# Kernel optimization log

Measured on AMD Instinct MI355X. Metric: run time of the kernel, lower is better.

The kernel has to match this reference:

```python
import jax, jax.numpy as jnp
import numpy as np

EPS = 1e-8  # torch F.cosine_similarity default eps


def setup_inputs() -> dict:
    key = jax.random.key(0)
    k1, k2 = jax.random.split(key)
    x = jax.random.normal(k1, (16384, 1024), dtype=jnp.float32)
    label = jax.random.randint(k2, (16384, 64), 0, 2).astype(jnp.int64)
    w = jnp.asarray(10.0, dtype=jnp.float32)  # nn.Parameter init_w
    b = jnp.asarray(-5.0, dtype=jnp.float32)  # nn.Parameter init_b
    return {"x": x, "label": label, "w": w, "b": b}


def reference(x, label, w, b):
    # Append the 'no-label' column for rows whose label vector is all zero.
    extra = (label.sum(axis=1) == 0).astype(label.dtype)[:, None]
    lab = jnp.concatenate([label, extra], axis=1).astype(x.dtype)  # [B, C]

    counts = lab.sum(axis=0)                  # [C] positives per centroid
    active = counts > 0                       # torch drops empty columns; we mask them

    # Centroids: mean of x over rows carrying each label (scatter-mean as GEMM).
    anchor = (lab.T @ x) / jnp.maximum(counts, 1.0)[:, None]   # [C, D]

    # Cosine similarity between every sample and every centroid.
    xn = jnp.maximum(jnp.linalg.norm(x, axis=1), EPS)          # [B]
    an = jnp.maximum(jnp.linalg.norm(anchor, axis=1), EPS)     # [C]
    cos = (x @ anchor.T) / (xn[:, None] * an[None, :])          # [B, C]

    logits = cos * w + b
    # Removing empty columns from softmax == setting their logits to -inf.
    logits = jnp.where(active[None, :], logits, -jnp.inf)
    logp = jax.nn.log_softmax(logits, axis=1)                   # [B, C]

    # Row expansion in torch duplicates sample i once per positive label j;
    # the logits row only depends on i, so CE over expanded rows is a
    # pair-weighted mean of -logp[i, j] over positive (i, j) pairs.
    n_pairs = lab.sum()
    nloss = -jnp.sum(jnp.where(lab > 0, logp, 0.0)) / n_pairs
    return nloss
```

## Files before the change

kernel.cpp:

```cpp
#include <hip/hip_runtime.h>
#include <hip/hip_bf16.h>
#include <stdint.h>

#define NROWS 16384
#define NDIM  1024
#define NLAB  64
#define NC    65
#define CPAD  80

typedef float float4v __attribute__((ext_vector_type(4)));
typedef short short8  __attribute__((ext_vector_type(8)));

static constexpr size_t SCALE_B = 0;
static constexpr size_t ACTB_B  = 320;
static constexpr size_t WSUM_B  = 400;
static constexpr size_t CNTF_B  = 448;
static constexpr size_t CNTP_B  = 1024;
static constexpr size_t MASK_B  = 83968;
static constexpr size_t XN2_B   = 215040;
static constexpr size_t LFRAG_B = 280576;
static constexpr size_t BFRAG_B = 2902016;
static constexpr size_t XAF_B   = 3065856;
static constexpr size_t PART_B  = 70174720;
static constexpr size_t SLAB    = (size_t)CPAD * NDIM * 4;
static constexpr size_t ANCH_SZ = (size_t)CPAD * NDIM * 4;
static constexpr size_t NRM_SZ  = (size_t)CPAD * 4 * 4;

__device__ __forceinline__ unsigned short bf16u(float f) {
    __hip_bfloat16 h = __float2bfloat16(f);
    return __builtin_bit_cast(unsigned short, h);
}
__device__ __forceinline__ unsigned pk2(float a, float b) {
    return (unsigned)bf16u(a) | ((unsigned)bf16u(b) << 16);
}

__global__ __launch_bounds__(256, 4) void k01_prep(const float* __restrict__ x,
                                                   const int* __restrict__ label,
                                                   unsigned short* __restrict__ xAfrag,
                                                   float* __restrict__ xn2g,
                                                   unsigned long long* __restrict__ masks,
                                                   unsigned* __restrict__ cntpart,
                                                   unsigned short* __restrict__ lfrag) {
    __shared__ unsigned cnt[NC];
    __shared__ unsigned long long smask[64];
    __shared__ float red[4][16];
    int t = threadIdx.x;
    if (blockIdx.x < 1024) {
        int rt = blockIdx.x;
        int w = t >> 6, lane = t & 63, q = lane >> 4, col = lane & 15;
        const float* rowp = x + ((size_t)rt * 16 + col) * NDIM;
        uint4* dst = (uint4*)xAfrag + ((size_t)rt * 32 + w * 8) * 64 + lane;
        float sq = 0.f;
#pragma unroll
        for (int kb = 0; kb < 8; ++kb) {
            int d0 = w * 256 + kb * 32 + q * 8;
            float4 fa = *(const float4*)(rowp + d0);
            float4 fb = *(const float4*)(rowp + d0 + 4);
            sq += fa.x * fa.x + fa.y * fa.y + fa.z * fa.z + fa.w * fa.w
                + fb.x * fb.x + fb.y * fb.y + fb.z * fb.z + fb.w * fb.w;
            uint4 v;
            v.x = pk2(fa.x, fa.y); v.y = pk2(fa.z, fa.w);
            v.z = pk2(fb.x, fb.y); v.w = pk2(fb.z, fb.w);
            dst[kb * 64] = v;
        }
        sq += __shfl_xor(sq, 16, 64);
        sq += __shfl_xor(sq, 32, 64);
        if (q == 0) red[w][col] = sq;
        __syncthreads();
        if (t < 16) xn2g[rt * 16 + t] = red[0][t] + red[1][t] + red[2][t] + red[3][t];
        return;
    }
    int bid = blockIdx.x - 1024;
    if (t < NC) cnt[t] = 0;
    __syncthreads();
    int wave = t >> 6, lane = t & 63;
    int rowblock = bid * 64;
    unsigned creg = 0, zreg = 0;
#pragma unroll 4
    for (int p = 0; p < 16; ++p) {
        int row = rowblock + p * 4 + wave;
        int v = label[row * NLAB + lane];
        unsigned long long m = __ballot(v != 0);
        creg += (unsigned)((m >> lane) & 1ull);
        if (lane == 0) {
            masks[row] = m;
            smask[p * 4 + wave] = m;
            zreg += (m == 0ull) ? 1u : 0u;
        }
    }
    atomicAdd(&cnt[lane], creg);
    if (lane == 0 && zreg) atomicAdd(&cnt[64], zreg);
    __syncthreads();
    if (t < 80) cntpart[bid * 80 + t] = (t < NC) ? cnt[t] : 0u;
    for (int pid = t; pid < 640; pid += 256) {
        int rt2l = pid / 320, rem = pid % 320;
        int ct = rem >> 6, ln = rem & 63;
        int q = ln >> 4, col = ln & 15;
        int c = ct * 16 + col;
        int rbase = rt2l * 32 + q * 8;
        unsigned pk[4];
#pragma unroll
        for (int jp = 0; jp < 4; ++jp) {
            unsigned long long m0 = smask[rbase + jp * 2], m1 = smask[rbase + jp * 2 + 1];
            unsigned b0, b1;
            if (c < 64)       { b0 = (unsigned)((m0 >> c) & 1ull); b1 = (unsigned)((m1 >> c) & 1ull); }
            else if (c == 64) { b0 = (m0 == 0ull); b1 = (m1 == 0ull); }
            else              { b0 = 0u; b1 = 0u; }
            pk[jp] = (b0 ? 0x3F80u : 0u) | (b1 ? 0x3F800000u : 0u);
        }
        uint4 w = make_uint4(pk[0], pk[1], pk[2], pk[3]);
        ((uint4*)lfrag)[((size_t)(bid * 2 + rt2l) * 5 + ct) * 64 + ln] = w;
    }
}

__global__ __launch_bounds__(256) void k2_sums(const float* __restrict__ x,
                                               const unsigned short* __restrict__ lfrag,
                                               float* __restrict__ partial,
                                               int kslices) {
    int t = threadIdx.x, wave = t >> 6, lane = t & 63;
    int q = lane >> 4, col = lane & 15;
    int dgroup = blockIdx.x & 15, ks = blockIdx.x >> 4;
    int nkb = (NROWS / kslices) >> 5;
    int kb0 = ks * nkb;
    int d = dgroup * 64 + wave * 16 + col;
    const uint4* A = (const uint4*)lfrag;
    const float* xb = x + d;

    float4v acc[5];
#pragma unroll
    for (int ct = 0; ct < 5; ++ct) acc[ct] = (float4v){0.f, 0.f, 0.f, 0.f};

    float f0[8], f1[8];
    uint4 a0[5], a1[5];
    {
        const float* p = xb + (size_t)(kb0 * 32 + q * 8) * NDIM;
#pragma unroll
        for (int j = 0; j < 8; ++j) f0[j] = p[(size_t)j * NDIM];
#pragma unroll
        for (int ct = 0; ct < 5; ++ct) a0[ct] = A[((size_t)kb0 * 5 + ct) * 64 + lane];
        const float* p1 = xb + (size_t)((kb0 + 1) * 32 + q * 8) * NDIM;
#pragma unroll
        for (int j = 0; j < 8; ++j) f1[j] = p1[(size_t)j * NDIM];
#pragma unroll
        for (int ct = 0; ct < 5; ++ct) a1[ct] = A[((size_t)(kb0 + 1) * 5 + ct) * 64 + lane];
    }

    for (int i = 0; i < nkb; i += 2) {
        int p2 = i + 2 < nkb ? kb0 + i + 2 : kb0 + i;
        int p3 = i + 3 < nkb ? kb0 + i + 3 : kb0 + i + 1;
        {
            uint4 bq;
            bq.x = pk2(f0[0], f0[1]); bq.y = pk2(f0[2], f0[3]);
            bq.z = pk2(f0[4], f0[5]); bq.w = pk2(f0[6], f0[7]);
            short8 bf = __builtin_bit_cast(short8, bq);
#pragma unroll
            for (int ct = 0; ct < 5; ++ct) {
                short8 af = __builtin_bit_cast(short8, a0[ct]);
                acc[ct] = __builtin_amdgcn_mfma_f32_16x16x32_bf16(af, bf, acc[ct], 0, 0, 0);
            }
            const float* p = xb + (size_t)(p2 * 32 + q * 8) * NDIM;
#pragma unroll
            for (int j = 0; j < 8; ++j) f0[j] = p[(size_t)j * NDIM];
#pragma unroll
            for (int ct = 0; ct < 5; ++ct) a0[ct] = A[((size_t)p2 * 5 + ct) * 64 + lane];
        }
        {
            uint4 bq;
            bq.x = pk2(f1[0], f1[1]); bq.y = pk2(f1[2], f1[3]);
            bq.z = pk2(f1[4], f1[5]); bq.w = pk2(f1[6], f1[7]);
            short8 bf = __builtin_bit_cast(short8, bq);
#pragma unroll
            for (int ct = 0; ct < 5; ++ct) {
                short8 af = __builtin_bit_cast(short8, a1[ct]);
                acc[ct] = __builtin_amdgcn_mfma_f32_16x16x32_bf16(af, bf, acc[ct], 0, 0, 0);
            }
            const float* p = xb + (size_t)(p3 * 32 + q * 8) * NDIM;
#pragma unroll
            for (int j = 0; j < 8; ++j) f1[j] = p[(size_t)j * NDIM];
#pragma unroll
            for (int ct = 0; ct < 5; ++ct) a1[ct] = A[((size_t)p3 * 5 + ct) * 64 + lane];
        }
    }
    float* pb = partial + (size_t)ks * CPAD * NDIM;
#pragma unroll
    for (int ct = 0; ct < 5; ++ct)
#pragma unroll
        for (int reg = 0; reg < 4; ++reg)
            pb[(size_t)(ct * 16 + q * 4 + reg) * NDIM + d] = acc[ct][reg];
}

__global__ __launch_bounds__(256) void k2bA(const float* __restrict__ partial,
                                            int kslices,
                                            float* __restrict__ anchor_raw,
                                            float* __restrict__ norm2part) {
    __shared__ float red[4];
    int c = blockIdx.x >> 2, dq = blockIdx.x & 3, t = threadIdx.x;
    int d = dq * 256 + t;
    const float* p = partial + (size_t)c * NDIM + d;
    float s = 0.f;
#pragma unroll 8
    for (int sl = 0; sl < kslices; ++sl) s += p[(size_t)sl * CPAD * NDIM];
    anchor_raw[(size_t)c * NDIM + d] = s;
    float ss = s * s;
#pragma unroll
    for (int m = 32; m >= 1; m >>= 1) ss += __shfl_xor(ss, m, 64);
    if ((t & 63) == 0) red[t >> 6] = ss;
    __syncthreads();
    if (t == 0) norm2part[blockIdx.x] = red[0] + red[1] + red[2] + red[3];
}

__global__ __launch_bounds__(1024) void k2bB(const float* __restrict__ wptr,
                                             const unsigned* __restrict__ cntpart,
                                             const float* __restrict__ anchor_raw,
                                             const float* __restrict__ norm2part,
                                             unsigned short* __restrict__ bfrag,
                                             float* __restrict__ scale,
                                             unsigned char* __restrict__ actB,
                                             unsigned* __restrict__ countsF,
                                             float* __restrict__ wsum) {
    int c = blockIdx.x, t = threadIdx.x;
    __shared__ float red[16];
    __shared__ unsigned credu[4];
    __shared__ float bcast[1];
    if (c == 0 && t == 512) *wsum = 0.f;
    if (t < 256) {
        unsigned cv = cntpart[t * 80 + c];
#pragma unroll
        for (int m = 32; m >= 1; m >>= 1) cv += __shfl_xor(cv, m, 64);
        if ((t & 63) == 0) credu[t >> 6] = cv;
    }
    if (t == 0)
        bcast[0] = sqrtf(norm2part[c * 4] + norm2part[c * 4 + 1] +
                         norm2part[c * 4 + 2] + norm2part[c * 4 + 3]);
    __syncthreads();
    unsigned cnt = credu[0] + credu[1] + credu[2] + credu[3];
    float invc = 1.0f / (float)(cnt > 0u ? cnt : 1u);
    float a = anchor_raw[(size_t)c * NDIM + t] * invc;
    float an = fmaxf(bcast[0] * invc, 1e-8f);
    unsigned short h = bf16u(a / an);
    int ct = c >> 4, colc = c & 15;
    int kb = t >> 5, q = (t >> 3) & 3, j0 = t & 7;
    bfrag[((((size_t)ct * 32 + kb) * 64) + q * 16 + colc) * 8 + j0] = h;
    float hv = __bfloat162float(__builtin_bit_cast(__hip_bfloat16, h));
    float nb2 = hv * hv;
#pragma unroll
    for (int m = 32; m >= 1; m >>= 1) nb2 += __shfl_xor(nb2, m, 64);
    if ((t & 63) == 0) red[t >> 6] = nb2;
    __syncthreads();
    if (t == 0) {
        float n2 = 0.f;
#pragma unroll
        for (int j = 0; j < 16; ++j) n2 += red[j];
        scale[c] = (n2 > 0.f) ? (wptr[0] / sqrtf(n2)) : 0.f;
        actB[c] = (cnt > 0u) ? 1 : 0;
        countsF[c] = cnt;
    }
}

__global__ __launch_bounds__(256) void k3_loss(const unsigned short* __restrict__ xAfrag,
                                               const unsigned short* __restrict__ bfrag,
                                               const float* __restrict__ xn2g,
                                               const unsigned long long* __restrict__ masks,
                                               const unsigned char* __restrict__ actB,
                                               const float* __restrict__ scale,
                                               const float* __restrict__ bptr,
                                               float* __restrict__ wsum) {
    __shared__ float redsm[3][64][21];
    int t = threadIdx.x, wave = t >> 6, lane = t & 63;
    int q = lane >> 4, col = lane & 15;
    int rt = blockIdx.x;
    int rowbase = rt * 16;
    const uint4* A = (const uint4*)xAfrag + (size_t)rt * 32 * 64 + lane;
    const uint4* Bp = (const uint4*)bfrag + lane;
    int kb0 = wave * 8;

    float4v acc[5];
#pragma unroll
    for (int ct = 0; ct < 5; ++ct) acc[ct] = (float4v){0.f, 0.f, 0.f, 0.f};

    uint4 a0 = A[(size_t)(kb0 + 0) * 64], a1 = A[(size_t)(kb0 + 1) * 64];
    uint4 b0[5], b1[5];
#pragma unroll
    for (int ct = 0; ct < 5; ++ct) b0[ct] = Bp[(size_t)(ct * 32 + kb0 + 0) * 64];
#pragma unroll
    for (int ct = 0; ct < 5; ++ct) b1[ct] = Bp[(size_t)(ct * 32 + kb0 + 1) * 64];

    for (int s = 0; s < 8; s += 2) {
        int p2 = s + 2 < 8 ? kb0 + s + 2 : kb0 + s;
        int p3 = s + 3 < 8 ? kb0 + s + 3 : kb0 + s + 1;
        {
            short8 af = __builtin_bit_cast(short8, a0);
#pragma unroll
            for (int ct = 0; ct < 5; ++ct) {
                short8 bf = __builtin_bit_cast(short8, b0[ct]);
                acc[ct] = __builtin_amdgcn_mfma_f32_16x16x32_bf16(af, bf, acc[ct], 0, 0, 0);
            }
            a0 = A[(size_t)p2 * 64];
#pragma unroll
            for (int ct = 0; ct < 5; ++ct) b0[ct] = Bp[(size_t)(ct * 32 + p2) * 64];
        }
        {
            short8 af = __builtin_bit_cast(short8, a1);
#pragma unroll
            for (int ct = 0; ct < 5; ++ct) {
                short8 bf = __builtin_bit_cast(short8, b1[ct]);
                acc[ct] = __builtin_amdgcn_mfma_f32_16x16x32_bf16(af, bf, acc[ct], 0, 0, 0);
            }
            a1 = A[(size_t)p3 * 64];
#pragma unroll
            for (int ct = 0; ct < 5; ++ct) b1[ct] = Bp[(size_t)(ct * 32 + p3) * 64];
        }
    }

    if (wave) {
#pragma unroll
        for (int ct = 0; ct < 5; ++ct)
#pragma unroll
            for (int reg = 0; reg < 4; ++reg)
                redsm[wave - 1][lane][ct * 4 + reg] = acc[ct][reg];
    }
    __syncthreads();
    if (wave != 0) return;
#pragma unroll
    for (int w = 0; w < 3; ++w)
#pragma unroll
        for (int ct = 0; ct < 5; ++ct)
#pragma unroll
            for (int reg = 0; reg < 4; ++reg)
                acc[ct][reg] += redsm[w][lane][ct * 4 + reg];

    float bv = bptr[0];
    float sc[5]; unsigned char ab[5];
#pragma unroll
    for (int ct = 0; ct < 5; ++ct) { sc[ct] = scale[ct * 16 + col]; ab[ct] = actB[ct * 16 + col]; }

    float contrib = 0.f;
#pragma unroll
    for (int reg = 0; reg < 4; ++reg) {
        int rl = q * 4 + reg;
        int row = rowbase + rl;
        float inv = 1.0f / fmaxf(sqrtf(xn2g[row]), 1e-8f);
        unsigned long long mask = masks[row];
        float v[5]; float lmax = -1e30f;
#pragma unroll
        for (int ct = 0; ct < 5; ++ct) {
            float lg = acc[ct][reg] * sc[ct] * inv + bv;
            v[ct] = ab[ct] ? lg : -1e30f;
            lmax = fmaxf(lmax, v[ct]);
        }
#pragma unroll
        for (int m = 1; m < 16; m <<= 1) lmax = fmaxf(lmax, __shfl_xor(lmax, m, 16));
        float es = 0.f;
#pragma unroll
        for (int ct = 0; ct < 5; ++ct) es += expf(v[ct] - lmax);
#pragma unroll
        for (int m = 1; m < 16; m <<= 1) es += __shfl_xor(es, m, 16);
        float lse = lmax + logf(es);
        float ps = 0.f;
#pragma unroll
        for (int ct = 0; ct < 5; ++ct) {
            int c = ct * 16 + col;
            bool pos = (c < 64) ? (((mask >> c) & 1ull) != 0ull)
                                : ((c == 64) ? (mask == 0ull) : false);
            ps += pos ? v[ct] : 0.f;
        }
#pragma unroll
        for (int m = 1; m < 16; m <<= 1) ps += __shfl_xor(ps, m, 16);
        float npos = mask ? (float)__popcll(mask) : 1.0f;
        float crow = ps - npos * lse;
        if (col == 0) contrib += crow;
    }
#pragma unroll
    for (int m = 1; m < 64; m <<= 1) contrib += __shfl_xor(contrib, m, 64);
    if (lane == 0) atomicAdd(wsum, contrib);
}

__global__ void k4_final(const unsigned* __restrict__ countsF,
                         const float* __restrict__ wsum,
                         float* __restrict__ out) {
    if (threadIdx.x == 0 && blockIdx.x == 0) {
        float np = 0.f;
        for (int c = 0; c < NC; ++c) np += (float)countsF[c];
        out[0] = -wsum[0] / np;
    }
}

extern "C" void kernel_launch(void* const* d_in, const int* in_sizes, int n_in,
                              void* d_out, int out_size, void* d_ws, size_t ws_size,
                              hipStream_t stream) {
    (void)in_sizes; (void)n_in; (void)out_size;
    const float* x = (const float*)d_in[0];
    const int* label = (const int*)d_in[1];
    const float* w = (const float*)d_in[2];
    const float* b = (const float*)d_in[3];

    char* ws = (char*)d_ws;
    float* scale = (float*)(ws + SCALE_B);
    unsigned char* actB = (unsigned char*)(ws + ACTB_B);
    float* wsum = (float*)(ws + WSUM_B);
    unsigned* countsF = (unsigned*)(ws + CNTF_B);
    unsigned* cntpart = (unsigned*)(ws + CNTP_B);
    unsigned long long* masks = (unsigned long long*)(ws + MASK_B);
    float* xn2g = (float*)(ws + XN2_B);
    unsigned short* lfrag = (unsigned short*)(ws + LFRAG_B);
    unsigned short* bfrag = (unsigned short*)(ws + BFRAG_B);
    unsigned short* xAfrag = (unsigned short*)(ws + XAF_B);
    float* partial = (float*)(ws + PART_B);

    int kslices = 64;
    while (kslices > 8 && PART_B + (size_t)kslices * SLAB + ANCH_SZ + NRM_SZ > ws_size)
        kslices >>= 1;
    float* anchor_raw = (float*)(ws + PART_B + (size_t)kslices * SLAB);
    float* norm2part = anchor_raw + CPAD * NDIM;

    hipLaunchKernelGGL(k01_prep, dim3(1024 + 256), dim3(256), 0, stream,
                       x, label, xAfrag, xn2g, masks, cntpart, lfrag);
    hipLaunchKernelGGL(k2_sums, dim3(16 * kslices), dim3(256), 0, stream,
                       x, lfrag, partial, kslices);
    hipLaunchKernelGGL(k2bA, dim3(CPAD * 4), dim3(256), 0, stream,
                       partial, kslices, anchor_raw, norm2part);
    hipLaunchKernelGGL(k2bB, dim3(CPAD), dim3(1024), 0, stream,
                       w, cntpart, anchor_raw, norm2part, bfrag, scale, actB, countsF, wsum);
    hipLaunchKernelGGL(k3_loss, dim3(NROWS / 16), dim3(256), 0, stream,
                       xAfrag, bfrag, xn2g, masks, actB, scale, b, wsum);
    hipLaunchKernelGGL(k4_final, dim3(1), dim3(64), 0, stream, countsF, wsum, (float*)d_out);
}
```

Baseline: 168.5 us.

## Fuse slice-reduction kernels, fold final into loss, stage x tile through LDS

Several independent changes land together. The two-stage partial reduction (k2bA + k2bB) becomes a single kC_fuse kernel. k4_final is folded into k3_loss with a last-block-done counter. kB_sums now loads x rows coalesced into a double-buffered LDS tile instead of issuing strided per-column global loads. The prep kernel batches all x loads before computing and drops its occupancy hint. These aim to cut launch count and uncoalesced traffic, at the cost of a per-iteration barrier in the sums loop and a serialized partial-sum read in the fused kernel (80 blocks each reading kslices slabs).

```diff
diff --git a/kernel.cpp b/kernel.cpp
--- a/kernel.cpp
+++ b/kernel.cpp
@@ -14,6 +14,7 @@
 static constexpr size_t SCALE_B = 0;
 static constexpr size_t ACTB_B  = 320;
 static constexpr size_t WSUM_B  = 400;
+static constexpr size_t DONE_B  = 404;
 static constexpr size_t CNTF_B  = 448;
 static constexpr size_t CNTP_B  = 1024;
 static constexpr size_t MASK_B  = 83968;
@@ -21,10 +22,8 @@
 static constexpr size_t LFRAG_B = 280576;
 static constexpr size_t BFRAG_B = 2902016;
 static constexpr size_t XAF_B   = 3065856;
-static constexpr size_t PART_B  = 70174720;
+static constexpr size_t PART_B  = 36620288;
 static constexpr size_t SLAB    = (size_t)CPAD * NDIM * 4;
-static constexpr size_t ANCH_SZ = (size_t)CPAD * NDIM * 4;
-static constexpr size_t NRM_SZ  = (size_t)CPAD * 4 * 4;
 
 __device__ __forceinline__ unsigned short bf16u(float f) {
     __hip_bfloat16 h = __float2bfloat16(f);
@@ -34,46 +33,50 @@
     return (unsigned)bf16u(a) | ((unsigned)bf16u(b) << 16);
 }
 
-__global__ __launch_bounds__(256, 4) void k01_prep(const float* __restrict__ x,
-                                                   const int* __restrict__ label,
-                                                   unsigned short* __restrict__ xAfrag,
-                                                   float* __restrict__ xn2g,
-                                                   unsigned long long* __restrict__ masks,
-                                                   unsigned* __restrict__ cntpart,
-                                                   unsigned short* __restrict__ lfrag) {
+__global__ __launch_bounds__(256) void kP_prep(const float* __restrict__ x,
+                                               const int* __restrict__ label,
+                                               unsigned short* __restrict__ xAfrag,
+                                               float* __restrict__ xn2g,
+                                               unsigned long long* __restrict__ masks,
+                                               unsigned* __restrict__ cntpart,
+                                               unsigned short* __restrict__ lfrag) {
+    __shared__ float red2[4][16];
     __shared__ unsigned cnt[NC];
     __shared__ unsigned long long smask[64];
-    __shared__ float red[4][16];
     int t = threadIdx.x;
+    int wave = t >> 6, lane = t & 63;
+    int q = lane >> 4, col = lane & 15;
     if (blockIdx.x < 1024) {
         int rt = blockIdx.x;
-        int w = t >> 6, lane = t & 63, q = lane >> 4, col = lane & 15;
         const float* rowp = x + ((size_t)rt * 16 + col) * NDIM;
-        uint4* dst = (uint4*)xAfrag + ((size_t)rt * 32 + w * 8) * 64 + lane;
+        uint4* dst = (uint4*)xAfrag + ((size_t)rt * 32 + wave * 8) * 64 + lane;
+        float4 fa[8], fb[8];
+#pragma unroll
+        for (int kb = 0; kb < 8; ++kb) {
+            int d0 = wave * 256 + kb * 32 + q * 8;
+            fa[kb] = *(const float4*)(rowp + d0);
+            fb[kb] = *(const float4*)(rowp + d0 + 4);
+        }
         float sq = 0.f;
 #pragma unroll
         for (int kb = 0; kb < 8; ++kb) {
-            int d0 = w * 256 + kb * 32 + q * 8;
-            float4 fa = *(const float4*)(rowp + d0);
-            float4 fb = *(const float4*)(rowp + d0 + 4);
-            sq += fa.x * fa.x + fa.y * fa.y + fa.z * fa.z + fa.w * fa.w
-                + fb.x * fb.x + fb.y * fb.y + fb.z * fb.z + fb.w * fb.w;
+            sq += fa[kb].x * fa[kb].x + fa[kb].y * fa[kb].y + fa[kb].z * fa[kb].z + fa[kb].w * fa[kb].w
+                + fb[kb].x * fb[kb].x + fb[kb].y * fb[kb].y + fb[kb].z * fb[kb].z + fb[kb].w * fb[kb].w;
             uint4 v;
-            v.x = pk2(fa.x, fa.y); v.y = pk2(fa.z, fa.w);
-            v.z = pk2(fb.x, fb.y); v.w = pk2(fb.z, fb.w);
+            v.x = pk2(fa[kb].x, fa[kb].y); v.y = pk2(fa[kb].z, fa[kb].w);
+            v.z = pk2(fb[kb].x, fb[kb].y); v.w = pk2(fb[kb].z, fb[kb].w);
             dst[kb * 64] = v;
         }
         sq += __shfl_xor(sq, 16, 64);
         sq += __shfl_xor(sq, 32, 64);
-        if (q == 0) red[w][col] = sq;
+        if (q == 0) red2[wave][col] = sq;
         __syncthreads();
-        if (t < 16) xn2g[rt * 16 + t] = red[0][t] + red[1][t] + red[2][t] + red[3][t];
+        if (t < 16) xn2g[rt * 16 + t] = red2[0][t] + red2[1][t] + red2[2][t] + red2[3][t];
         return;
     }
     int bid = blockIdx.x - 1024;
     if (t < NC) cnt[t] = 0;
     __syncthreads();
-    int wave = t >> 6, lane = t & 63;
     int rowblock = bid * 64;
     unsigned creg = 0, zreg = 0;
 #pragma unroll 4
@@ -95,9 +98,9 @@
     for (int pid = t; pid < 640; pid += 256) {
         int rt2l = pid / 320, rem = pid % 320;
         int ct = rem >> 6, ln = rem & 63;
-        int q = ln >> 4, col = ln & 15;
-        int c = ct * 16 + col;
-        int rbase = rt2l * 32 + q * 8;
+        int qq = ln >> 4, cc = ln & 15;
+        int c = ct * 16 + cc;
+        int rbase = rt2l * 32 + qq * 8;
         unsigned pk[4];
 #pragma unroll
         for (int jp = 0; jp < 4; ++jp) {
@@ -113,10 +116,11 @@
     }
 }
 
-__global__ __launch_bounds__(256) void k2_sums(const float* __restrict__ x,
+__global__ __launch_bounds__(256) void kB_sums(const float* __restrict__ x,
                                                const unsigned short* __restrict__ lfrag,
                                                float* __restrict__ partial,
                                                int kslices) {
+    __shared__ float xt[2][32][65];
     int t = threadIdx.x, wave = t >> 6, lane = t & 63;
     int q = lane >> 4, col = lane & 15;
     int dgroup = blockIdx.x & 15, ks = blockIdx.x >> 4;
@@ -124,62 +128,51 @@
     int kb0 = ks * nkb;
     int d = dgroup * 64 + wave * 16 + col;
     const uint4* A = (const uint4*)lfrag;
-    const float* xb = x + d;
+    int srow = t >> 3, sd = (t & 7) * 8;
 
     float4v acc[5];
 #pragma unroll
     for (int ct = 0; ct < 5; ++ct) acc[ct] = (float4v){0.f, 0.f, 0.f, 0.f};
 
-    float f0[8], f1[8];
-    uint4 a0[5], a1[5];
     {
-        const float* p = xb + (size_t)(kb0 * 32 + q * 8) * NDIM;
-#pragma unroll
-        for (int j = 0; j < 8; ++j) f0[j] = p[(size_t)j * NDIM];
-#pragma unroll
-        for (int ct = 0; ct < 5; ++ct) a0[ct] = A[((size_t)kb0 * 5 + ct) * 64 + lane];
-        const float* p1 = xb + (size_t)((kb0 + 1) * 32 + q * 8) * NDIM;
-#pragma unroll
-        for (int j = 0; j < 8; ++j) f1[j] = p1[(size_t)j * NDIM];
-#pragma unroll
-        for (int ct = 0; ct < 5; ++ct) a1[ct] = A[((size_t)(kb0 + 1) * 5 + ct) * 64 + lane];
-    }
-
-    for (int i = 0; i < nkb; i += 2) {
-        int p2 = i + 2 < nkb ? kb0 + i + 2 : kb0 + i;
-        int p3 = i + 3 < nkb ? kb0 + i + 3 : kb0 + i + 1;
-        {
-            uint4 bq;
-            bq.x = pk2(f0[0], f0[1]); bq.y = pk2(f0[2], f0[3]);
-            bq.z = pk2(f0[4], f0[5]); bq.w = pk2(f0[6], f0[7]);
-            short8 bf = __builtin_bit_cast(short8, bq);
-#pragma unroll
-            for (int ct = 0; ct < 5; ++ct) {
-                short8 af = __builtin_bit_cast(short8, a0[ct]);
-                acc[ct] = __builtin_amdgcn_mfma_f32_16x16x32_bf16(af, bf, acc[ct], 0, 0, 0);
-            }
-            const float* p = xb + (size_t)(p2 * 32 + q * 8) * NDIM;
-#pragma unroll
-            for (int j = 0; j < 8; ++j) f0[j] = p[(size_t)j * NDIM];
-#pragma unroll
-            for (int ct = 0; ct < 5; ++ct) a0[ct] = A[((size_t)p2 * 5 + ct) * 64 + lane];
-        }
-        {
-            uint4 bq;
-            bq.x = pk2(f1[0], f1[1]); bq.y = pk2(f1[2], f1[3]);
-            bq.z = pk2(f1[4], f1[5]); bq.w = pk2(f1[6], f1[7]);
-            short8 bf = __builtin_bit_cast(short8, bq);
-#pragma unroll
-            for (int ct = 0; ct < 5; ++ct) {
-                short8 af = __builtin_bit_cast(short8, a1[ct]);
-                acc[ct] = __builtin_amdgcn_mfma_f32_16x16x32_bf16(af, bf, acc[ct], 0, 0, 0);
-            }
-            const float* p = xb + (size_t)(p3 * 32 + q * 8) * NDIM;
-#pragma unroll
-            for (int j = 0; j < 8; ++j) f1[j] = p[(size_t)j * NDIM];
-#pragma unroll
-            for (int ct = 0; ct < 5; ++ct) a1[ct] = A[((size_t)p3 * 5 + ct) * 64 + lane];
-        }
+        const float* g = x + ((size_t)(kb0 * 32 + srow)) * NDIM + dgroup * 64 + sd;
+        float4 u = *(const float4*)g, v2 = *(const float4*)(g + 4);
+        float* L = &xt[0][srow][sd];
+        L[0] = u.x; L[1] = u.y; L[2] = u.z; L[3] = u.w;
+        L[4] = v2.x; L[5] = v2.y; L[6] = v2.z; L[7] = v2.w;
+    }
+    __syncthreads();
+
+    for (int i = 0; i < nkb; ++i) {
+        int cur = i & 1;
+        float4 u, v2;
+        bool havenext = (i + 1) < nkb;
+        if (havenext) {
+            const float* g = x + ((size_t)((kb0 + i + 1) * 32 + srow)) * NDIM + dgroup * 64 + sd;
+            u = *(const float4*)g; v2 = *(const float4*)(g + 4);
+        }
+        int kb = kb0 + i;
+        uint4 a0[5];
+#pragma unroll
+        for (int ct = 0; ct < 5; ++ct) a0[ct] = A[((size_t)kb * 5 + ct) * 64 + lane];
+        float f[8];
+#pragma unroll
+        for (int j = 0; j < 8; ++j) f[j] = xt[cur][q * 8 + j][wave * 16 + col];
+        uint4 bq;
+        bq.x = pk2(f[0], f[1]); bq.y = pk2(f[2], f[3]);
+        bq.z = pk2(f[4], f[5]); bq.w = pk2(f[6], f[7]);
+        short8 bf = __builtin_bit_cast(short8, bq);
+#pragma unroll
+        for (int ct = 0; ct < 5; ++ct) {
+            short8 af = __builtin_bit_cast(short8, a0[ct]);
+            acc[ct] = __builtin_amdgcn_mfma_f32_16x16x32_bf16(af, bf, acc[ct], 0, 0, 0);
+        }
+        if (havenext) {
+            float* L = &xt[cur ^ 1][srow][sd];
+            L[0] = u.x; L[1] = u.y; L[2] = u.z; L[3] = u.w;
+            L[4] = v2.x; L[5] = v2.y; L[6] = v2.z; L[7] = v2.w;
+        }
+        __syncthreads();
     }
     float* pb = partial + (size_t)ks * CPAD * NDIM;
 #pragma unroll
@@ -189,53 +182,47 @@
             pb[(size_t)(ct * 16 + q * 4 + reg) * NDIM + d] = acc[ct][reg];
 }
 
-__global__ __launch_bounds__(256) void k2bA(const float* __restrict__ partial,
-                                            int kslices,
-                                            float* __restrict__ anchor_raw,
-                                            float* __restrict__ norm2part) {
-    __shared__ float red[4];
-    int c = blockIdx.x >> 2, dq = blockIdx.x & 3, t = threadIdx.x;
-    int d = dq * 256 + t;
-    const float* p = partial + (size_t)c * NDIM + d;
-    float s = 0.f;
-#pragma unroll 8
-    for (int sl = 0; sl < kslices; ++sl) s += p[(size_t)sl * CPAD * NDIM];
-    anchor_raw[(size_t)c * NDIM + d] = s;
-    float ss = s * s;
-#pragma unroll
-    for (int m = 32; m >= 1; m >>= 1) ss += __shfl_xor(ss, m, 64);
-    if ((t & 63) == 0) red[t >> 6] = ss;
-    __syncthreads();
-    if (t == 0) norm2part[blockIdx.x] = red[0] + red[1] + red[2] + red[3];
-}
-
-__global__ __launch_bounds__(1024) void k2bB(const float* __restrict__ wptr,
-                                             const unsigned* __restrict__ cntpart,
-                                             const float* __restrict__ anchor_raw,
-                                             const float* __restrict__ norm2part,
-                                             unsigned short* __restrict__ bfrag,
-                                             float* __restrict__ scale,
-                                             unsigned char* __restrict__ actB,
-                                             unsigned* __restrict__ countsF,
-                                             float* __restrict__ wsum) {
+__global__ __launch_bounds__(1024) void kC_fuse(const float* __restrict__ wptr,
+                                                const unsigned* __restrict__ cntpart,
+                                                const float* __restrict__ partial,
+                                                int kslices,
+                                                unsigned short* __restrict__ bfrag,
+                                                float* __restrict__ scale,
+                                                unsigned char* __restrict__ actB,
+                                                unsigned* __restrict__ countsF,
+                                                float* __restrict__ wsum,
+                                                unsigned* __restrict__ done) {
     int c = blockIdx.x, t = threadIdx.x;
     __shared__ float red[16];
     __shared__ unsigned credu[4];
     __shared__ float bcast[1];
     if (c == 0 && t == 512) *wsum = 0.f;
+    if (c == 0 && t == 513) *done = 0u;
     if (t < 256) {
         unsigned cv = cntpart[t * 80 + c];
 #pragma unroll
         for (int m = 32; m >= 1; m >>= 1) cv += __shfl_xor(cv, m, 64);
         if ((t & 63) == 0) credu[t >> 6] = cv;
     }
-    if (t == 0)
-        bcast[0] = sqrtf(norm2part[c * 4] + norm2part[c * 4 + 1] +
-                         norm2part[c * 4 + 2] + norm2part[c * 4 + 3]);
-    __syncthreads();
+    const float* p = partial + (size_t)c * NDIM + t;
+    float s = 0.f;
+#pragma unroll 8
+    for (int sl = 0; sl < kslices; ++sl) s += p[(size_t)sl * CPAD * NDIM];
+    float ss = s * s;
+#pragma unroll
+    for (int m = 32; m >= 1; m >>= 1) ss += __shfl_xor(ss, m, 64);
+    if ((t & 63) == 0) red[t >> 6] = ss;
+    __syncthreads();
+    if (t == 0) {
+        float tot = 0.f;
+#pragma unroll
+        for (int j = 0; j < 16; ++j) tot += red[j];
+        bcast[0] = sqrtf(tot);
+    }
     unsigned cnt = credu[0] + credu[1] + credu[2] + credu[3];
+    __syncthreads();
     float invc = 1.0f / (float)(cnt > 0u ? cnt : 1u);
-    float a = anchor_raw[(size_t)c * NDIM + t] * invc;
+    float a = s * invc;
     float an = fmaxf(bcast[0] * invc, 1e-8f);
     unsigned short h = bf16u(a / an);
     int ct = c >> 4, colc = c & 15;
@@ -264,7 +251,10 @@
                                                const unsigned char* __restrict__ actB,
                                                const float* __restrict__ scale,
                                                const float* __restrict__ bptr,
-                                               float* __restrict__ wsum) {
+                                               float* __restrict__ wsum,
+                                               unsigned* __restrict__ done,
+                                               const unsigned* __restrict__ countsF,
+                                               float* __restrict__ out) {
     __shared__ float redsm[3][64][21];
     int t = threadIdx.x, wave = t >> 6, lane = t & 63;
     int q = lane >> 4, col = lane & 15;
@@ -372,16 +362,17 @@
     }
 #pragma unroll
     for (int m = 1; m < 64; m <<= 1) contrib += __shfl_xor(contrib, m, 64);
-    if (lane == 0) atomicAdd(wsum, contrib);
-}
-
-__global__ void k4_final(const unsigned* __restrict__ countsF,
-                         const float* __restrict__ wsum,
-                         float* __restrict__ out) {
-    if (threadIdx.x == 0 && blockIdx.x == 0) {
-        float np = 0.f;
-        for (int c = 0; c < NC; ++c) np += (float)countsF[c];
-        out[0] = -wsum[0] / np;
+    if (lane == 0) {
+        atomicAdd(wsum, contrib);
+        __threadfence();
+        unsigned prev = atomicAdd(done, 1u);
+        if (prev == (unsigned)gridDim.x - 1u) {
+            __threadfence();
+            float wv = __hip_atomic_load(wsum, __ATOMIC_ACQUIRE, __HIP_MEMORY_SCOPE_AGENT);
+            float np = 0.f;
+            for (int c = 0; c < NC; ++c) np += (float)countsF[c];
+            out[0] = -wv / np;
+        }
     }
 }
 
@@ -398,6 +389,7 @@
     float* scale = (float*)(ws + SCALE_B);
     unsigned char* actB = (unsigned char*)(ws + ACTB_B);
     float* wsum = (float*)(ws + WSUM_B);
+    unsigned* done = (unsigned*)(ws + DONE_B);
     unsigned* countsF = (unsigned*)(ws + CNTF_B);
     unsigned* cntpart = (unsigned*)(ws + CNTP_B);
     unsigned long long* masks = (unsigned long long*)(ws + MASK_B);
@@ -408,20 +400,14 @@
     float* partial = (float*)(ws + PART_B);
 
     int kslices = 64;
-    while (kslices > 8 && PART_B + (size_t)kslices * SLAB + ANCH_SZ + NRM_SZ > ws_size)
-        kslices >>= 1;
-    float* anchor_raw = (float*)(ws + PART_B + (size_t)kslices * SLAB);
-    float* norm2part = anchor_raw + CPAD * NDIM;
-
-    hipLaunchKernelGGL(k01_prep, dim3(1024 + 256), dim3(256), 0, stream,
+    while (kslices > 8 && PART_B + (size_t)kslices * SLAB > ws_size) kslices >>= 1;
+
+    hipLaunchKernelGGL(kP_prep, dim3(1024 + 256), dim3(256), 0, stream,
                        x, label, xAfrag, xn2g, masks, cntpart, lfrag);
-    hipLaunchKernelGGL(k2_sums, dim3(16 * kslices), dim3(256), 0, stream,
+    hipLaunchKernelGGL(kB_sums, dim3(16 * kslices), dim3(256), 0, stream,
                        x, lfrag, partial, kslices);
-    hipLaunchKernelGGL(k2bA, dim3(CPAD * 4), dim3(256), 0, stream,
-                       partial, kslices, anchor_raw, norm2part);
-    hipLaunchKernelGGL(k2bB, dim3(CPAD), dim3(1024), 0, stream,
-                       w, cntpart, anchor_raw, norm2part, bfrag, scale, actB, countsF, wsum);
+    hipLaunchKernelGGL(kC_fuse, dim3(CPAD), dim3(1024), 0, stream,
+                       w, cntpart, partial, kslices, bfrag, scale, actB, countsF, wsum, done);
     hipLaunchKernelGGL(k3_loss, dim3(NROWS / 16), dim3(256), 0, stream,
-                       xAfrag, bfrag, xn2g, masks, actB, scale, b, wsum);
-    hipLaunchKernelGGL(k4_final, dim3(1), dim3(64), 0, stream, countsF, wsum, (float*)d_out);
-}
+                       xAfrag, bfrag, xn2g, masks, actB, scale, b, wsum, done, countsF, (float*)d_out);
+}
```

After: 176.5 us. +4.7%, slower.
